# Optimization experiments

Measured on AMD Instinct MI355X. Metric: run time of the kernel, lower is better.

Reference implementation:

```python
import jax, jax.numpy as jnp
import numpy as np
from jax import lax

B, T, F = 64, 100, 128
HD = [32, 64]            # encoder hidden dims; decoder uses reversed [64, 32]
KH, KW = 3, 3


def _conv(x, w):
    # x: (b, cin, f, 1), w: (cout, cin, kh, kw), SAME padding
    ph, pw = w.shape[2] // 2, w.shape[3] // 2
    return lax.conv_general_dilated(x, w, (1, 1), [(ph, ph), (pw, pw)],
                                    dimension_numbers=("NCHW", "OIHW", "NCHW"))


def _run_layer(xs, h0, wg, bg, wc, bc):
    # xs: (t, b, cin, f, 1); h0: (b, hd, f, 1)
    def step(h, x):
        g = _conv(jnp.concatenate([x, h], axis=1), wg) + bg[None, :, None, None]
        r, u = jnp.split(jax.nn.sigmoid(g), 2, axis=1)
        c = jnp.tanh(_conv(jnp.concatenate([x, r * h], axis=1), wc) + bc[None, :, None, None])
        h_next = (1.0 - u) * h + u * c
        return h_next, h_next
    h_last, ys = lax.scan(step, h0, xs)
    return ys, h_last


def setup_inputs() -> dict:
    key = jax.random.key(0)
    ks = iter(jax.random.split(key, 32))
    s = 0.05
    d = {"x": jax.random.normal(next(ks), (B, T, F), dtype=jnp.float32)}
    # encoder: layer0 in=1 hd=32, layer1 in=32 hd=64
    # decoder: input_dim=64, hidden reversed [64,32]: layer0 in=64 hd=64, layer1 in=64 hd=32
    specs = {
        "e0": (1, 32), "e1": (32, 64),
        "d0": (64, 64), "d1": (64, 32),
    }
    for name, (cin, hd) in specs.items():
        d[name + "_wg"] = jax.random.normal(next(ks), (2 * hd, cin + hd, KH, KW), dtype=jnp.float32) * s
        d[name + "_bg"] = jnp.zeros((2 * hd,), dtype=jnp.float32)
        d[name + "_wc"] = jax.random.normal(next(ks), (hd, cin + hd, KH, KW), dtype=jnp.float32) * s
        d[name + "_bc"] = jnp.zeros((hd,), dtype=jnp.float32)
    d["fw"] = jax.random.normal(next(ks), (1, 32, 1, 1), dtype=jnp.float32) * s
    d["fb"] = jnp.zeros((1,), dtype=jnp.float32)
    return d


def reference(x,
              e0_wg, e0_bg, e0_wc, e0_bc,
              e1_wg, e1_bg, e1_wc, e1_bc,
              d0_wg, d0_bg, d0_wc, d0_bc,
              d1_wg, d1_bg, d1_wc, d1_bc,
              fw, fb):
    b, t, f = x.shape
    xs = x.reshape(b, t, 1, f, 1).transpose(1, 0, 2, 3, 4)  # (t,b,1,f,1)
    zeros = lambda hd: jnp.zeros((b, hd, f, 1), dtype=x.dtype)
    # encoder (return_all_layers; decoder consumes last layer output)
    y0, h0 = _run_layer(xs, zeros(HD[0]), e0_wg, e0_bg, e0_wc, e0_bc)
    y1, h1 = _run_layer(y0, zeros(HD[1]), e1_wg, e1_bg, e1_wc, e1_bc)
    # decoder init states = encoder last states reversed: [h1 (64ch), h0 (32ch)]
    z0, _ = _run_layer(y1, h1, d0_wg, d0_bg, d0_wc, d0_bc)
    z1, _ = _run_layer(z0, h0, d1_wg, d1_bg, d1_wc, d1_bc)
    # final 1x1 conv: (t,b,32,f,1) x (1,32) -> (t,b,1,f,1)
    rec = jnp.einsum("tbcfw,oc->tbofw", z1, fw[:, :, 0, 0]) + fb[None, None, :, None, None]
    return rec.transpose(1, 0, 2, 3, 4).reshape(b, t, f)
```

## Files before the change

### kernel.cpp

```cpp
#include <hip/hip_runtime.h>
#include <cstdint>
#include <cstddef>


#define F_ 128
#define T_ 100
#define B_ 64
#define ROWSP 130
#define CBSTR (ROWSP * 8)
#define CBBYTE (ROWSP * 16)
#define AT_OFF 104448
#define LDS_TOTAL (AT_OFF + 28 * CBBYTE)

typedef _Float16 f16;
typedef __attribute__((ext_vector_type(4))) float f32x4;
typedef __attribute__((ext_vector_type(8))) _Float16 f16x8;
typedef __attribute__((ext_vector_type(4))) _Float16 f16x4;

#define MFMA(a, b, c) __builtin_amdgcn_mfma_f32_16x16x32_f16(a, b, c, 0, 0, 0)

__device__ __forceinline__ float exp2_(float x) { return __builtin_amdgcn_exp2f(x); }
__device__ __forceinline__ float rcp_(float x) { return __builtin_amdgcn_rcpf(x); }

#define KSG (-1.442695041f)
#define KTH (-2.885390082f)

__host__ __device__ constexpr int cbA(int lid, int km) {
  return lid == 0 ? (km ? 4 : 0)
       : lid == 1 ? (1 + km * 4)
       : lid == 2 ? (km * 4)
                  : (8 + km * 4);
}
__host__ __device__ constexpr int cbB(int lid, int km) {
  return lid == 0 ? (km ? 17 : 13)
       : lid == 1 ? (km == 0 ? 1 : 14 + km * 4)
       : lid == 2 ? (km < 2 ? km * 4 : 12 + km * 4)
                  : (km < 2 ? 8 + km * 4 : 20);
}

template <int LID, int NCR, int NK, int NC3, int HC, int RHC,
          bool GREG, bool CREG, bool EMITY1>
__device__ __forceinline__ void gru_layer(
    const f16* __restrict__ rdB, char* __restrict__ wrB,
    const f16x8* __restrict__ aR, const f16x8* __restrict__ aU,
    const f16* __restrict__ gR, const f16* __restrict__ gU,
    const f16x8* __restrict__ cR, const f16* __restrict__ cW,
    const f32x4 bR2, const f32x4 bU2, const f32x4 bC2,
    f32x4* __restrict__ hreg, f16* __restrict__ y1dst) {
  constexpr int FTW = NCR;
  f32x4 accR[FTW], accU[FTW];
#pragma unroll
  for (int j = 0; j < FTW; ++j) {
    accR[j] = (f32x4){0.f, 0.f, 0.f, 0.f};
    accU[j] = (f32x4){0.f, 0.f, 0.f, 0.f};
  }
#pragma unroll
  for (int ks = 0; ks < NK; ++ks) {
    const int k = ks / NC3, km = ks % NC3;
    const f16* fb = rdB + cbA(LID, km) * CBSTR + k * 8;
    f16x8 bf[FTW];
#pragma unroll
    for (int j = 0; j < FTW; ++j) bf[j] = *(const f16x8*)(fb + j * 128);
    f16x8 wr, wu;
    if constexpr (GREG) {
      wr = aR[ks];
      wu = aU[ks];
    } else {
      wr = *(const f16x8*)(gR + ks * 512);
      wu = *(const f16x8*)(gU + ks * 512);
    }
#pragma unroll
    for (int j = 0; j < FTW; ++j) accR[j] = MFMA(wr, bf[j], accR[j]);
#pragma unroll
    for (int j = 0; j < FTW; ++j) accU[j] = MFMA(wu, bf[j], accU[j]);
  }
#pragma unroll
  for (int j = 0; j < FTW; ++j) {
    f16x4 rh;
#pragma unroll
    for (int q = 0; q < 4; ++q) {
      const float r = rcp_(1.0f + exp2_(fmaf(accR[j][q], KSG, bR2[q])));
      rh[q] = (f16)(r * hreg[j][q]);
    }
    *(f16x4*)(wrB + (RHC >> 3) * CBBYTE + j * 256) = rh;
  }
  __syncthreads();
  f32x4 accC[FTW];
#pragma unroll
  for (int j = 0; j < FTW; ++j) accC[j] = (f32x4){0.f, 0.f, 0.f, 0.f};
#pragma unroll
  for (int ks = 0; ks < NK; ++ks) {
    const int k = ks / NC3, km = ks % NC3;
    const f16* fb = rdB + cbB(LID, km) * CBSTR + k * 8;
    f16x8 bf[FTW];
#pragma unroll
    for (int j = 0; j < FTW; ++j) bf[j] = *(const f16x8*)(fb + j * 128);
    f16x8 wc;
    if constexpr (CREG) wc = cR[ks];
    else wc = *(const f16x8*)(cW + ks * 512);
#pragma unroll
    for (int j = 0; j < FTW; ++j) accC[j] = MFMA(wc, bf[j], accC[j]);
  }
#pragma unroll
  for (int j = 0; j < FTW; ++j) {
    f16x4 hh;
#pragma unroll
    for (int q = 0; q < 4; ++q) {
      const float u = rcp_(1.0f + exp2_(fmaf(accU[j][q], KSG, bU2[q])));
      const float r = rcp_(1.0f + exp2_(fmaf(accC[j][q], KTH, bC2[q])));
      const float h = hreg[j][q];
      const float s = fmaf(2.0f, r, -(1.0f + h));
      const float hn = fmaf(u, s, h);
      hreg[j][q] = hn;
      hh[q] = (f16)hn;
    }
    *(f16x4*)(wrB + (HC >> 3) * CBBYTE + j * 256) = hh;
    if constexpr (EMITY1) *(f16x4*)(y1dst + j * 128) = hh;
  }
}

__global__ __launch_bounds__(512, 1) void ae_kernel(
    const f16* __restrict__ xf, float* __restrict__ out,
    const f16* __restrict__ wgE0, const f16* __restrict__ wcE0,
    const float* __restrict__ bgE0, const float* __restrict__ bcE0,
    const f16* __restrict__ wgE1, const f16* __restrict__ wcE1,
    const float* __restrict__ bgE1, const float* __restrict__ bcE1,
    const f16* __restrict__ wgD0, const f16* __restrict__ wcD0,
    const float* __restrict__ bgD0, const float* __restrict__ bcD0,
    const f16* __restrict__ wgD1, const f16* __restrict__ wcD1,
    const float* __restrict__ bgD1, const float* __restrict__ bcD1,
    const float* __restrict__ fw, const float* __restrict__ fb,
    f16* __restrict__ y1g) {
  extern __shared__ char smem[];
  f16* aT = (f16*)(smem + AT_OFF);
  const int tid = threadIdx.x, b = blockIdx.x;
  const int w = tid >> 6, l = tid & 63;
  const int m16 = l & 15, kb = l >> 4;

  for (int i = tid; i < 28 * CBBYTE / 16; i += 512)
    ((f32x4*)(smem + AT_OFF))[i] = (f32x4){0.f, 0.f, 0.f, 0.f};
  for (int i = tid; i < 1536; i += 512)
    ((f16x8*)(smem + 0))[i] = ((const f16x8*)wgE0)[i];
  for (int i = tid; i < 768; i += 512)
    ((f16x8*)(smem + 24576))[i] = ((const f16x8*)wcE0)[i];

  const int cot2 = w & 1, cot4 = w & 3;
  f16x8 aR1[9], aU1[9], cE1[9];
#pragma unroll
  for (int ks = 0; ks < 9; ++ks) {
    aR1[ks] = ((const f16x8*)wgE1)[(cot4 * 9 + ks) * 64 + l];
    aU1[ks] = ((const f16x8*)wgE1)[((cot4 + 4) * 9 + ks) * 64 + l];
    cE1[ks] = ((const f16x8*)wcE1)[(cot4 * 9 + ks) * 64 + l];
  }
  const int co2 = cot2 * 16 + kb * 4;
  const int co4 = cot4 * 16 + kb * 4;
  f32x4 bRe0, bUe0, bCe0, bRe1, bUe1, bCe1;
#pragma unroll
  for (int q = 0; q < 4; ++q) {
    bRe0[q] = bgE0[co2 + q] * KSG;
    bUe0[q] = bgE0[32 + co2 + q] * KSG;
    bCe0[q] = bcE0[co2 + q] * KTH;
    bRe1[q] = bgE1[co4 + q] * KSG;
    bUe1[q] = bgE1[64 + co4 + q] * KSG;
    bCe1[q] = bcE1[co4 + q] * KTH;
  }
  const int ft2 = (w >> 1) * 2, ft4 = (w >> 2) * 4;
  const f16* rdB2 = aT + kb * CBSTR + (ft2 * 16 + m16) * 8;
  const f16* rdB4 = aT + kb * CBSTR + (ft4 * 16 + m16) * 8;
  char* wrB2 = (char*)aT + (cot2 * 2 + (kb >> 1)) * CBBYTE +
               (ft2 * 16 + m16 + 1) * 16 + (kb & 1) * 8;
  char* wrB4 = (char*)aT + (cot4 * 2 + (kb >> 1)) * CBBYTE +
               (ft4 * 16 + m16 + 1) * 16 + (kb & 1) * 8;
  f16* y1t = y1g + (size_t)b * T_ * 8192 +
             ((cot4 * 2 + (kb >> 1)) * 128 + ft4 * 16 + m16) * 8 + (kb & 1) * 4;
  const f16* gE0R = (const f16*)(smem + 0) + (cot2 * 6) * 512 + l * 8;
  const f16* gE0U = (const f16*)(smem + 0) + ((2 + cot2) * 6) * 512 + l * 8;
  const f16* cE0 = (const f16*)(smem + 24576) + (cot2 * 6) * 512 + l * 8;

  f32x4 h0r[2], h1r[4];
#pragma unroll
  for (int j = 0; j < 2; ++j) h0r[j] = (f32x4){0.f, 0.f, 0.f, 0.f};
#pragma unroll
  for (int j = 0; j < 4; ++j) h1r[j] = (f32x4){0.f, 0.f, 0.f, 0.f};
  __syncthreads();

  const f16* xb = xf + (size_t)b * T_ * F_;
  for (int t = 0; t < T_; ++t) {
    if (tid < F_) {
      const f16 v = xb[t * F_ + tid];
      aT[(tid + 1) * 8] = v;
      aT[13 * CBSTR + (tid + 1) * 8] = v;
    }
    __syncthreads();
    gru_layer<0, 2, 6, 2, 8, 112, false, false, false>(
        rdB2, wrB2, nullptr, nullptr, gE0R, gE0U, nullptr, cE0,
        bRe0, bUe0, bCe0, h0r, nullptr);
    __syncthreads();
    gru_layer<1, 4, 9, 3, 40, 144, true, true, true>(
        rdB4, wrB4, aR1, aU1, nullptr, nullptr, cE1, nullptr,
        bRe1, bUe1, bCe1, h1r, y1t + t * 8192);
    __syncthreads();
  }

  {
#pragma unroll
    for (int j = 0; j < 4; ++j) {
      f16x4 hh;
#pragma unroll
      for (int q = 0; q < 4; ++q) hh[q] = (f16)h1r[j][q];
      *(f16x4*)(wrB4 + 8 * CBBYTE + j * 256) = hh;
    }
#pragma unroll
    for (int j = 0; j < 2; ++j) {
      f16x4 hh;
#pragma unroll
      for (int q = 0; q < 4; ++q) hh[q] = (f16)h0r[j][q];
      *(f16x4*)(wrB2 + 16 * CBBYTE + j * 256) = hh;
    }
  }
  for (int i = tid; i < 3072; i += 512)
    ((f16x8*)(smem + 0))[i] = ((const f16x8*)wcD0)[i];
  for (int i = tid; i < 2304; i += 512)
    ((f16x8*)(smem + 49152))[i] = ((const f16x8*)wgD1)[i];
  for (int i = tid; i < 1152; i += 512)
    ((f16x8*)(smem + 86016))[i] = ((const f16x8*)wcD1)[i];
  f16x8 aR0[12], aU0[12];
#pragma unroll
  for (int ks = 0; ks < 12; ++ks) {
    aR0[ks] = ((const f16x8*)wgD0)[(cot4 * 12 + ks) * 64 + l];
    aU0[ks] = ((const f16x8*)wgD0)[((cot4 + 4) * 12 + ks) * 64 + l];
  }
  f32x4 bRd0, bUd0, bCd0, bRd1, bUd1, bCd1;
#pragma unroll
  for (int q = 0; q < 4; ++q) {
    bRd0[q] = bgD0[co4 + q] * KSG;
    bUd0[q] = bgD0[64 + co4 + q] * KSG;
    bCd0[q] = bcD0[co4 + q] * KTH;
    bRd1[q] = bgD1[co2 + q] * KSG;
    bUd1[q] = bgD1[32 + co2 + q] * KSG;
    bCd1[q] = bcD1[co2 + q] * KTH;
  }
  const f16* cD0 = (const f16*)(smem + 0) + (cot4 * 12) * 512 + l * 8;
  const f16* gD1R = (const f16*)(smem + 49152) + (cot2 * 9) * 512 + l * 8;
  const f16* gD1U = (const f16*)(smem + 49152) + ((2 + cot2) * 9) * 512 + l * 8;
  const f16* cD1 = (const f16*)(smem + 86016) + (cot2 * 9) * 512 + l * 8;
  __syncthreads();

  for (int t = 0; t < T_; ++t) {
    {
      const f16x8* src = (const f16x8*)(y1g + ((size_t)b * T_ + t) * 8192);
#pragma unroll
      for (int k2 = 0; k2 < 2; ++k2) {
        const int i = tid + k2 * 512;
        *(f16x8*)&aT[(i >> 7) * CBSTR + ((i & 127) + 1) * 8] = src[i];
      }
    }
    __syncthreads();
    gru_layer<2, 4, 12, 4, 64, 160, true, false, false>(
        rdB4, wrB4, aR0, aU0, nullptr, nullptr, nullptr, cD0,
        bRd0, bUd0, bCd0, h1r, nullptr);
    __syncthreads();
    gru_layer<3, 2, 9, 3, 128, 160, false, false, false>(
        rdB2, wrB2, nullptr, nullptr, gD1R, gD1U, nullptr, cD1,
        bRd1, bUd1, bCd1, h0r, nullptr);
    __syncthreads();
    if (tid < F_) {
      float s = fb[0];
#pragma unroll
      for (int cb = 0; cb < 4; ++cb) {
        const f16x8 h8 = *(const f16x8*)&aT[(16 + cb) * CBSTR + (tid + 1) * 8];
#pragma unroll
        for (int q = 0; q < 8; ++q) s = fmaf(fw[cb * 8 + q], (float)h8[q], s);
      }
      out[((size_t)b * T_ + t) * F_ + tid] = s;
    }
  }
}

__global__ void repack_f16(const float* __restrict__ src, f16* __restrict__ dst,
                           int CO, int CI, int CINH, int NK, int e0map) {
  const int n = (CO / 16) * NK * 64;
  for (int i = blockIdx.x * blockDim.x + threadIdx.x; i < n;
       i += gridDim.x * blockDim.x) {
    const int cot = i / (NK * 64);
    const int r = i - cot * NK * 64;
    const int ks = r >> 6, lph = r & 63;
    const int co = cot * 16 + (lph & 15);
    const int kbl = lph >> 4;
#pragma unroll
    for (int j = 0; j < 8; ++j) {
      const int kk = ks * 32 + kbl * 8 + j;
      const int k = kk / CINH, c = kk - k * CINH;
      int ci;
      if (e0map) ci = (c == 0) ? 0 : ((c >= 8 && c < 40) ? c - 7 : -1);
      else ci = (c < CI) ? c : -1;
      float wv = 0.f;
      if (ci >= 0) wv = src[((size_t)(co * CI + ci) * 3 + k) * 3 + 1];
      dst[(size_t)i * 8 + j] = (f16)wv;
    }
  }
}

__global__ void xcvt(const float* __restrict__ x, f16* __restrict__ xf, int n4) {
  for (int i = blockIdx.x * blockDim.x + threadIdx.x; i < n4;
       i += gridDim.x * blockDim.x) {
    const float4 v = ((const float4*)x)[i];
    f16x4 o;
    o[0] = (f16)v.x; o[1] = (f16)v.y; o[2] = (f16)v.z; o[3] = (f16)v.w;
    ((f16x4*)xf)[i] = o;
  }
}

extern "C" void kernel_launch(void* const* d_in, const int* in_sizes, int n_in,
                              void* d_out, int out_size, void* d_ws, size_t ws_size,
                              hipStream_t stream) {
  (void)in_sizes; (void)n_in; (void)out_size; (void)ws_size;
  const float* x = (const float*)d_in[0];
  const float* e0_wg = (const float*)d_in[1];
  const float* e0_bg = (const float*)d_in[2];
  const float* e0_wc = (const float*)d_in[3];
  const float* e0_bc = (const float*)d_in[4];
  const float* e1_wg = (const float*)d_in[5];
  const float* e1_bg = (const float*)d_in[6];
  const float* e1_wc = (const float*)d_in[7];
  const float* e1_bc = (const float*)d_in[8];
  const float* d0_wg = (const float*)d_in[9];
  const float* d0_bg = (const float*)d_in[10];
  const float* d0_wc = (const float*)d_in[11];
  const float* d0_bc = (const float*)d_in[12];
  const float* d1_wg = (const float*)d_in[13];
  const float* d1_bg = (const float*)d_in[14];
  const float* d1_wc = (const float*)d_in[15];
  const float* d1_bc = (const float*)d_in[16];
  const float* fw = (const float*)d_in[17];
  const float* fb = (const float*)d_in[18];
  float* out = (float*)d_out;

  char* p = (char*)d_ws;
  f16* y1g = (f16*)p;
  p += (size_t)B_ * T_ * 64 * 128 * 2;
  f16* xf = (f16*)p;
  p += (size_t)B_ * T_ * F_ * 2;
  auto aw = [&](int n) { f16* q = (f16*)p; p += (size_t)n * 2; return q; };
  f16* wgE0 = aw(64 * 192);
  f16* wcE0 = aw(32 * 192);
  f16* wgE1 = aw(128 * 288);
  f16* wcE1 = aw(64 * 288);
  f16* wgD0 = aw(128 * 384);
  f16* wcD0 = aw(64 * 384);
  f16* wgD1 = aw(64 * 288);
  f16* wcD1 = aw(32 * 288);

  auto rp = [&](const float* s, f16* d, int CO, int CI, int CINH, int e0m) {
    const int NK = 3 * CINH / 32;
    const int n = (CO / 16) * NK * 64;
    hipLaunchKernelGGL(repack_f16, dim3((n + 255) / 256), dim3(256), 0, stream,
                       s, d, CO, CI, CINH, NK, e0m);
  };
  rp(e0_wg, wgE0, 64, 33, 64, 1);
  rp(e0_wc, wcE0, 32, 33, 64, 1);
  rp(e1_wg, wgE1, 128, 96, 96, 0);
  rp(e1_wc, wcE1, 64, 96, 96, 0);
  rp(d0_wg, wgD0, 128, 128, 128, 0);
  rp(d0_wc, wcD0, 64, 128, 128, 0);
  rp(d1_wg, wgD1, 64, 96, 96, 0);
  rp(d1_wc, wcD1, 32, 96, 96, 0);
  hipLaunchKernelGGL(xcvt, dim3(200), dim3(1024), 0, stream, x, xf,
                     B_ * T_ * F_ / 4);

  hipFuncSetAttribute((const void*)ae_kernel,
                      hipFuncAttributeMaxDynamicSharedMemorySize, LDS_TOTAL);
  hipLaunchKernelGGL(ae_kernel, dim3(B_), dim3(512), LDS_TOTAL, stream, xf, out,
                     wgE0, wcE0, e0_bg, e0_bc, wgE1, wcE1, e1_bg, e1_bc,
                     wgD0, wcD0, d0_bg, d0_bc, wgD1, wcD1, d1_bg, d1_bc,
                     fw, fb, y1g);
}
```

Before: 1.247 ms.

## Wavefront-pipeline stacked GRU layers across timesteps to cut barriers per step

Restructures both the encoder and decoder loops so layer 0 at step i and layer 1 at step i-1 run in the same iteration. Their gate convolutions, post-processing and candidate convolutions now share barriers, giving three barriers per combined step instead of about five or six. This needs a new LDS channel-block layout (NCB=32, AT_OFF moved) so the two layers' r*h and h buffers do not collide. The decoder candidate weights move from LDS into registers, and the final 1x1 projection is folded into the pipelined loop. The cost is higher register pressure and an extra pipeline fill and drain iteration.

```diff
diff --git a/kernel.cpp b/kernel.cpp
--- a/kernel.cpp
+++ b/kernel.cpp
@@ -9,8 +9,9 @@
 #define ROWSP 130
 #define CBSTR (ROWSP * 8)
 #define CBBYTE (ROWSP * 16)
-#define AT_OFF 104448
-#define LDS_TOTAL (AT_OFF + 28 * CBBYTE)
+#define AT_OFF 86016
+#define NCB 32
+#define LDS_TOTAL (AT_OFF + NCB * CBBYTE)
 
 typedef _Float16 f16;
 typedef __attribute__((ext_vector_type(4))) float f32x4;
@@ -35,20 +36,15 @@
   return lid == 0 ? (km ? 17 : 13)
        : lid == 1 ? (km == 0 ? 1 : 14 + km * 4)
        : lid == 2 ? (km < 2 ? km * 4 : 12 + km * 4)
-                  : (km < 2 ? 8 + km * 4 : 20);
-}
-
-template <int LID, int NCR, int NK, int NC3, int HC, int RHC,
-          bool GREG, bool CREG, bool EMITY1>
-__device__ __forceinline__ void gru_layer(
-    const f16* __restrict__ rdB, char* __restrict__ wrB,
+                  : (km < 2 ? 8 + km * 4 : 28);
+}
+
+template <int LID, int FTW, int NK, int NC3, bool WREG>
+__device__ __forceinline__ void convA_f(
+    const f16* __restrict__ rdB,
     const f16x8* __restrict__ aR, const f16x8* __restrict__ aU,
     const f16* __restrict__ gR, const f16* __restrict__ gU,
-    const f16x8* __restrict__ cR, const f16* __restrict__ cW,
-    const f32x4 bR2, const f32x4 bU2, const f32x4 bC2,
-    f32x4* __restrict__ hreg, f16* __restrict__ y1dst) {
-  constexpr int FTW = NCR;
-  f32x4 accR[FTW], accU[FTW];
+    f32x4* __restrict__ accR, f32x4* __restrict__ accU) {
 #pragma unroll
   for (int j = 0; j < FTW; ++j) {
     accR[j] = (f32x4){0.f, 0.f, 0.f, 0.f};
@@ -62,10 +58,8 @@
 #pragma unroll
     for (int j = 0; j < FTW; ++j) bf[j] = *(const f16x8*)(fb + j * 128);
     f16x8 wr, wu;
-    if constexpr (GREG) {
-      wr = aR[ks];
-      wu = aU[ks];
-    } else {
+    if constexpr (WREG) { wr = aR[ks]; wu = aU[ks]; }
+    else {
       wr = *(const f16x8*)(gR + ks * 512);
       wu = *(const f16x8*)(gU + ks * 512);
     }
@@ -74,18 +68,12 @@
 #pragma unroll
     for (int j = 0; j < FTW; ++j) accU[j] = MFMA(wu, bf[j], accU[j]);
   }
-#pragma unroll
-  for (int j = 0; j < FTW; ++j) {
-    f16x4 rh;
-#pragma unroll
-    for (int q = 0; q < 4; ++q) {
-      const float r = rcp_(1.0f + exp2_(fmaf(accR[j][q], KSG, bR2[q])));
-      rh[q] = (f16)(r * hreg[j][q]);
-    }
-    *(f16x4*)(wrB + (RHC >> 3) * CBBYTE + j * 256) = rh;
-  }
-  __syncthreads();
-  f32x4 accC[FTW];
+}
+
+template <int LID, int FTW, int NK, int NC3, bool CREG>
+__device__ __forceinline__ void convB_f(
+    const f16* __restrict__ rdB, const f16x8* __restrict__ cR,
+    const f16* __restrict__ cW, f32x4* __restrict__ accC) {
 #pragma unroll
   for (int j = 0; j < FTW; ++j) accC[j] = (f32x4){0.f, 0.f, 0.f, 0.f};
 #pragma unroll
@@ -101,20 +89,46 @@
 #pragma unroll
     for (int j = 0; j < FTW; ++j) accC[j] = MFMA(wc, bf[j], accC[j]);
   }
+}
+
+template <int FTW, int RHCB>
+__device__ __forceinline__ void postA_f(const f32x4* __restrict__ accR,
+                                        const f32x4 bR,
+                                        const f32x4* __restrict__ hreg,
+                                        char* __restrict__ wrB) {
+#pragma unroll
+  for (int j = 0; j < FTW; ++j) {
+    f16x4 rh;
+#pragma unroll
+    for (int q = 0; q < 4; ++q) {
+      const float r = rcp_(1.0f + exp2_(fmaf(accR[j][q], KSG, bR[q])));
+      rh[q] = (f16)(r * hreg[j][q]);
+    }
+    *(f16x4*)(wrB + RHCB * CBBYTE + j * 256) = rh;
+  }
+}
+
+template <int FTW, int HCB, bool EMITY1>
+__device__ __forceinline__ void postB_f(const f32x4* __restrict__ accU,
+                                        const f32x4* __restrict__ accC,
+                                        const f32x4 bU, const f32x4 bC,
+                                        f32x4* __restrict__ hreg,
+                                        char* __restrict__ wrB,
+                                        f16* __restrict__ y1dst) {
 #pragma unroll
   for (int j = 0; j < FTW; ++j) {
     f16x4 hh;
 #pragma unroll
     for (int q = 0; q < 4; ++q) {
-      const float u = rcp_(1.0f + exp2_(fmaf(accU[j][q], KSG, bU2[q])));
-      const float r = rcp_(1.0f + exp2_(fmaf(accC[j][q], KTH, bC2[q])));
+      const float u = rcp_(1.0f + exp2_(fmaf(accU[j][q], KSG, bU[q])));
+      const float r = rcp_(1.0f + exp2_(fmaf(accC[j][q], KTH, bC[q])));
       const float h = hreg[j][q];
       const float s = fmaf(2.0f, r, -(1.0f + h));
       const float hn = fmaf(u, s, h);
       hreg[j][q] = hn;
       hh[q] = (f16)hn;
     }
-    *(f16x4*)(wrB + (HC >> 3) * CBBYTE + j * 256) = hh;
+    *(f16x4*)(wrB + HCB * CBBYTE + j * 256) = hh;
     if constexpr (EMITY1) *(f16x4*)(y1dst + j * 128) = hh;
   }
 }
@@ -137,7 +151,7 @@
   const int w = tid >> 6, l = tid & 63;
   const int m16 = l & 15, kb = l >> 4;
 
-  for (int i = tid; i < 28 * CBBYTE / 16; i += 512)
+  for (int i = tid; i < NCB * CBBYTE / 16; i += 512)
     ((f32x4*)(smem + AT_OFF))[i] = (f32x4){0.f, 0.f, 0.f, 0.f};
   for (int i = tid; i < 1536; i += 512)
     ((f16x8*)(smem + 0))[i] = ((const f16x8*)wgE0)[i];
@@ -145,12 +159,12 @@
     ((f16x8*)(smem + 24576))[i] = ((const f16x8*)wcE0)[i];
 
   const int cot2 = w & 1, cot4 = w & 3;
-  f16x8 aR1[9], aU1[9], cE1[9];
+  f16x8 wR1[9], wU1[9], wC1[9];
 #pragma unroll
   for (int ks = 0; ks < 9; ++ks) {
-    aR1[ks] = ((const f16x8*)wgE1)[(cot4 * 9 + ks) * 64 + l];
-    aU1[ks] = ((const f16x8*)wgE1)[((cot4 + 4) * 9 + ks) * 64 + l];
-    cE1[ks] = ((const f16x8*)wcE1)[(cot4 * 9 + ks) * 64 + l];
+    wR1[ks] = ((const f16x8*)wgE1)[(cot4 * 9 + ks) * 64 + l];
+    wU1[ks] = ((const f16x8*)wgE1)[((cot4 + 4) * 9 + ks) * 64 + l];
+    wC1[ks] = ((const f16x8*)wcE1)[(cot4 * 9 + ks) * 64 + l];
   }
   const int co2 = cot2 * 16 + kb * 4;
   const int co4 = cot4 * 16 + kb * 4;
@@ -175,7 +189,7 @@
              ((cot4 * 2 + (kb >> 1)) * 128 + ft4 * 16 + m16) * 8 + (kb & 1) * 4;
   const f16* gE0R = (const f16*)(smem + 0) + (cot2 * 6) * 512 + l * 8;
   const f16* gE0U = (const f16*)(smem + 0) + ((2 + cot2) * 6) * 512 + l * 8;
-  const f16* cE0 = (const f16*)(smem + 24576) + (cot2 * 6) * 512 + l * 8;
+  const f16* cE0l = (const f16*)(smem + 24576) + (cot2 * 6) * 512 + l * 8;
 
   f32x4 h0r[2], h1r[4];
 #pragma unroll
@@ -185,20 +199,33 @@
   __syncthreads();
 
   const f16* xb = xf + (size_t)b * T_ * F_;
-  for (int t = 0; t < T_; ++t) {
-    if (tid < F_) {
-      const f16 v = xb[t * F_ + tid];
+  if (tid < F_) {
+    const f16 v = xb[tid];
+    aT[(tid + 1) * 8] = v;
+    aT[13 * CBSTR + (tid + 1) * 8] = v;
+  }
+  __syncthreads();
+  for (int i = 0; i <= T_; ++i) {
+    f32x4 aR0g[2], aU0g[2], aR1g[4], aU1g[4];
+    if (i < T_) convA_f<0, 2, 6, 2, false>(rdB2, nullptr, nullptr, gE0R, gE0U,
+                                           aR0g, aU0g);
+    if (i > 0) convA_f<1, 4, 9, 3, true>(rdB4, wR1, wU1, nullptr, nullptr,
+                                         aR1g, aU1g);
+    if (i < T_) postA_f<2, 14>(aR0g, bRe0, h0r, wrB2);
+    if (i > 0) postA_f<4, 18>(aR1g, bRe1, h1r, wrB4);
+    __syncthreads();
+    f32x4 aC0[2], aC1[4];
+    if (i < T_) convB_f<0, 2, 6, 2, false>(rdB2, nullptr, cE0l, aC0);
+    if (i > 0) convB_f<1, 4, 9, 3, true>(rdB4, wC1, nullptr, aC1);
+    __syncthreads();
+    if (i < T_) postB_f<2, 1, false>(aU0g, aC0, bUe0, bCe0, h0r, wrB2, nullptr);
+    if (i > 0) postB_f<4, 5, true>(aU1g, aC1, bUe1, bCe1, h1r, wrB4,
+                                   y1t + (size_t)(i - 1) * 8192);
+    if (i + 1 < T_ && tid < F_) {
+      const f16 v = xb[(i + 1) * F_ + tid];
       aT[(tid + 1) * 8] = v;
       aT[13 * CBSTR + (tid + 1) * 8] = v;
     }
-    __syncthreads();
-    gru_layer<0, 2, 6, 2, 8, 112, false, false, false>(
-        rdB2, wrB2, nullptr, nullptr, gE0R, gE0U, nullptr, cE0,
-        bRe0, bUe0, bCe0, h0r, nullptr);
-    __syncthreads();
-    gru_layer<1, 4, 9, 3, 40, 144, true, true, true>(
-        rdB4, wrB4, aR1, aU1, nullptr, nullptr, cE1, nullptr,
-        bRe1, bUe1, bCe1, h1r, y1t + t * 8192);
     __syncthreads();
   }
 
@@ -222,14 +249,15 @@
     ((f16x8*)(smem + 0))[i] = ((const f16x8*)wcD0)[i];
   for (int i = tid; i < 2304; i += 512)
     ((f16x8*)(smem + 49152))[i] = ((const f16x8*)wgD1)[i];
-  for (int i = tid; i < 1152; i += 512)
-    ((f16x8*)(smem + 86016))[i] = ((const f16x8*)wcD1)[i];
-  f16x8 aR0[12], aU0[12];
+  f16x8 wRd0[12], wUd0[12], wCd1[9];
 #pragma unroll
   for (int ks = 0; ks < 12; ++ks) {
-    aR0[ks] = ((const f16x8*)wgD0)[(cot4 * 12 + ks) * 64 + l];
-    aU0[ks] = ((const f16x8*)wgD0)[((cot4 + 4) * 12 + ks) * 64 + l];
-  }
+    wRd0[ks] = ((const f16x8*)wgD0)[(cot4 * 12 + ks) * 64 + l];
+    wUd0[ks] = ((const f16x8*)wgD0)[((cot4 + 4) * 12 + ks) * 64 + l];
+  }
+#pragma unroll
+  for (int ks = 0; ks < 9; ++ks)
+    wCd1[ks] = ((const f16x8*)wcD1)[(cot2 * 9 + ks) * 64 + l];
   f32x4 bRd0, bUd0, bCd0, bRd1, bUd1, bCd1;
 #pragma unroll
   for (int q = 0; q < 4; ++q) {
@@ -240,40 +268,56 @@
     bUd1[q] = bgD1[32 + co2 + q] * KSG;
     bCd1[q] = bcD1[co2 + q] * KTH;
   }
-  const f16* cD0 = (const f16*)(smem + 0) + (cot4 * 12) * 512 + l * 8;
+  const f16* cD0l = (const f16*)(smem + 0) + (cot4 * 12) * 512 + l * 8;
   const f16* gD1R = (const f16*)(smem + 49152) + (cot2 * 9) * 512 + l * 8;
   const f16* gD1U = (const f16*)(smem + 49152) + ((2 + cot2) * 9) * 512 + l * 8;
-  const f16* cD1 = (const f16*)(smem + 86016) + (cot2 * 9) * 512 + l * 8;
+  const float fb0 = fb[0];
   __syncthreads();
-
-  for (int t = 0; t < T_; ++t) {
-    {
-      const f16x8* src = (const f16x8*)(y1g + ((size_t)b * T_ + t) * 8192);
-#pragma unroll
-      for (int k2 = 0; k2 < 2; ++k2) {
-        const int i = tid + k2 * 512;
-        *(f16x8*)&aT[(i >> 7) * CBSTR + ((i & 127) + 1) * 8] = src[i];
-      }
-    }
-    __syncthreads();
-    gru_layer<2, 4, 12, 4, 64, 160, true, false, false>(
-        rdB4, wrB4, aR0, aU0, nullptr, nullptr, nullptr, cD0,
-        bRd0, bUd0, bCd0, h1r, nullptr);
-    __syncthreads();
-    gru_layer<3, 2, 9, 3, 128, 160, false, false, false>(
-        rdB2, wrB2, nullptr, nullptr, gD1R, gD1U, nullptr, cD1,
-        bRd1, bUd1, bCd1, h0r, nullptr);
-    __syncthreads();
-    if (tid < F_) {
-      float s = fb[0];
+  {
+    const f16x8* src = (const f16x8*)(y1g + (size_t)b * T_ * 8192);
+#pragma unroll
+    for (int k2 = 0; k2 < 2; ++k2) {
+      const int i = tid + k2 * 512;
+      *(f16x8*)&aT[(i >> 7) * CBSTR + ((i & 127) + 1) * 8] = src[i];
+    }
+  }
+  __syncthreads();
+
+  for (int i = 0; i <= T_ + 1; ++i) {
+    f32x4 aRd0[4], aUd0[4], aRd1[2], aUd1[2];
+    if (i < T_) convA_f<2, 4, 12, 4, true>(rdB4, wRd0, wUd0, nullptr, nullptr,
+                                           aRd0, aUd0);
+    if (i >= 1 && i <= T_)
+      convA_f<3, 2, 9, 3, false>(rdB2, nullptr, nullptr, gD1R, gD1U, aRd1, aUd1);
+    if (i >= 2 && tid < F_) {
+      float s = fb0;
 #pragma unroll
       for (int cb = 0; cb < 4; ++cb) {
         const f16x8 h8 = *(const f16x8*)&aT[(16 + cb) * CBSTR + (tid + 1) * 8];
 #pragma unroll
         for (int q = 0; q < 8; ++q) s = fmaf(fw[cb * 8 + q], (float)h8[q], s);
       }
-      out[((size_t)b * T_ + t) * F_ + tid] = s;
-    }
+      out[((size_t)b * T_ + (i - 2)) * F_ + tid] = s;
+    }
+    if (i < T_) postA_f<4, 20>(aRd0, bRd0, h1r, wrB4);
+    if (i >= 1 && i <= T_) postA_f<2, 28>(aRd1, bRd1, h0r, wrB2);
+    __syncthreads();
+    f32x4 aCd0[4], aCd1[2];
+    if (i < T_) convB_f<2, 4, 12, 4, false>(rdB4, nullptr, cD0l, aCd0);
+    if (i >= 1 && i <= T_) convB_f<3, 2, 9, 3, true>(rdB2, wCd1, nullptr, aCd1);
+    __syncthreads();
+    if (i < T_) postB_f<4, 8, false>(aUd0, aCd0, bUd0, bCd0, h1r, wrB4, nullptr);
+    if (i >= 1 && i <= T_)
+      postB_f<2, 16, false>(aUd1, aCd1, bUd1, bCd1, h0r, wrB2, nullptr);
+    if (i + 1 < T_) {
+      const f16x8* src = (const f16x8*)(y1g + ((size_t)b * T_ + (i + 1)) * 8192);
+#pragma unroll
+      for (int k2 = 0; k2 < 2; ++k2) {
+        const int idx = tid + k2 * 512;
+        *(f16x8*)&aT[(idx >> 7) * CBSTR + ((idx & 127) + 1) * 8] = src[idx];
+      }
+    }
+    __syncthreads();
   }
 }
 
```

Measured after the change: 1.459 ms. +17.0%, slower.
